# Kernel tuning notes

Hardware: AMD Instinct MI355X
Metric: run time of the kernel (lower is better)

The kernel has to match this reference:

```python
import jax, jax.numpy as jnp
import numpy as np

NUM_GRAPHS = 512  # batch_size (number of segments)


def setup_inputs() -> dict:
    key = jax.random.key(0)
    k1, k2 = jax.random.split(key)
    x = jax.random.normal(k1, (200000, 256), dtype=jnp.float32)
    batch = jnp.sort(jax.random.randint(k2, (200000,), 0, NUM_GRAPHS, dtype=jnp.int64))
    return {"x": x, "batch": batch}


def reference(x, batch):
    # scatter-add node features into per-graph sums: out[g] = sum_{i: batch[i]==g} x[i]
    return jax.ops.segment_sum(x, batch, num_segments=NUM_GRAPHS)
```

## Files before the change

kernel.cpp:

```cpp
#include <hip/hip_runtime.h>


#define FEAT 256
#define F4   (FEAT / 4)
#define NSEG 512

__global__ void seg_bounds_kernel(const int* __restrict__ batch,
                                  int* __restrict__ start, int n) {
    int r = blockIdx.x * blockDim.x + threadIdx.x;
    if (r >= n) return;
    int cur = batch[r];
    if (r == 0) {
        for (int g = 0; g <= cur; ++g) start[g] = 0;
    } else {
        int prev = batch[r - 1];
        for (int g = prev + 1; g <= cur; ++g) start[g] = r;
    }
    if (r == n - 1) {
        for (int g = cur + 1; g <= NSEG; ++g) start[g] = n;
    }
}

__global__ __launch_bounds__(256) void GraphAddPooling_39539468927441_kernel(
    const float* __restrict__ x, const int* __restrict__ start,
    float* __restrict__ out)
{
    const int g    = blockIdx.x;
    const int lane = threadIdx.x & 63;
    const int wave = threadIdx.x >> 6;

    const int r0 = start[g];
    const int r1 = start[g + 1];

    const float4* __restrict__ x4 = (const float4*)x;

    float4 a0 = make_float4(0.f, 0.f, 0.f, 0.f);
    float4 a1 = a0, a2 = a0, a3 = a0;

    int r = r0 + wave;
    for (; r + 12 < r1; r += 16) {
        float4 v0 = x4[(size_t)r        * F4 + lane];
        float4 v1 = x4[(size_t)(r + 4)  * F4 + lane];
        float4 v2 = x4[(size_t)(r + 8)  * F4 + lane];
        float4 v3 = x4[(size_t)(r + 12) * F4 + lane];
        a0.x += v0.x; a0.y += v0.y; a0.z += v0.z; a0.w += v0.w;
        a1.x += v1.x; a1.y += v1.y; a1.z += v1.z; a1.w += v1.w;
        a2.x += v2.x; a2.y += v2.y; a2.z += v2.z; a2.w += v2.w;
        a3.x += v3.x; a3.y += v3.y; a3.z += v3.z; a3.w += v3.w;
    }
    for (; r < r1; r += 4) {
        float4 v = x4[(size_t)r * F4 + lane];
        a0.x += v.x; a0.y += v.y; a0.z += v.z; a0.w += v.w;
    }
    a0.x += a1.x + a2.x + a3.x;
    a0.y += a1.y + a2.y + a3.y;
    a0.z += a1.z + a2.z + a3.z;
    a0.w += a1.w + a2.w + a3.w;

    __shared__ float4 red[4][F4];
    red[wave][lane] = a0;
    __syncthreads();
    if (wave == 0) {
        float4 s = red[0][lane];
        float4 b = red[1][lane], c = red[2][lane], d = red[3][lane];
        s.x += b.x + c.x + d.x;
        s.y += b.y + c.y + d.y;
        s.z += b.z + c.z + d.z;
        s.w += b.w + c.w + d.w;
        ((float4*)out)[(size_t)g * F4 + lane] = s;
    }
}

extern "C" void kernel_launch(void* const* d_in, const int* in_sizes, int n_in,
                              void* d_out, int out_size, void* d_ws, size_t ws_size,
                              hipStream_t stream) {
    const float* x     = (const float*)d_in[0];
    const int*   batch = (const int*)d_in[1];
    float*       out   = (float*)d_out;
    int*         start = (int*)d_ws;

    const int n_rows = in_sizes[1];

    seg_bounds_kernel<<<(n_rows + 255) / 256, 256, 0, stream>>>(batch, start, n_rows);
    GraphAddPooling_39539468927441_kernel<<<NSEG, 256, 0, stream>>>(x, start, out);
}
```

Measured before the change: 282.0 us.

## Split rows evenly across blocks and combine segment partials with atomics

Replaces the one-block-per-segment schedule with a fixed grid of 1024 blocks, each covering an equal contiguous range of rows. Within its range a block walks the segments it overlaps and accumulates each one per wave, adding the partial sums into the output with float atomics after zeroing the output with a memset. The aim is balanced work and more blocks in flight than the 512 segments allowed. In exchange it adds a memset, atomic traffic (four atomics per lane per wave per segment), and a summation order that is no longer deterministic.

```diff
diff --git a/kernel.cpp b/kernel.cpp
--- a/kernel.cpp
+++ b/kernel.cpp
@@ -4,6 +4,7 @@
 #define FEAT 256
 #define F4   (FEAT / 4)
 #define NSEG 512
+#define NB   1024
 
 __global__ void seg_bounds_kernel(const int* __restrict__ batch,
                                   int* __restrict__ start, int n) {
@@ -22,52 +23,56 @@
 }
 
 __global__ __launch_bounds__(256) void GraphAddPooling_39539468927441_kernel(
-    const float* __restrict__ x, const int* __restrict__ start,
-    float* __restrict__ out)
+    const float* __restrict__ x, const int* __restrict__ batch,
+    const int* __restrict__ start, float* __restrict__ out,
+    int n, int rows_per_block)
 {
-    const int g    = blockIdx.x;
     const int lane = threadIdx.x & 63;
     const int wave = threadIdx.x >> 6;
 
-    const int r0 = start[g];
-    const int r1 = start[g + 1];
+    const int c0 = blockIdx.x * rows_per_block;
+    if (c0 >= n) return;
+    int c1 = c0 + rows_per_block;
+    if (c1 > n) c1 = n;
 
     const float4* __restrict__ x4 = (const float4*)x;
 
-    float4 a0 = make_float4(0.f, 0.f, 0.f, 0.f);
-    float4 a1 = a0, a2 = a0, a3 = a0;
+    int g = batch[c0];
+    int r = c0;
+    while (r < c1) {
+        while (start[g + 1] <= r) ++g;
+        int rend = start[g + 1];
+        if (rend > c1) rend = c1;
 
-    int r = r0 + wave;
-    for (; r + 12 < r1; r += 16) {
-        float4 v0 = x4[(size_t)r        * F4 + lane];
-        float4 v1 = x4[(size_t)(r + 4)  * F4 + lane];
-        float4 v2 = x4[(size_t)(r + 8)  * F4 + lane];
-        float4 v3 = x4[(size_t)(r + 12) * F4 + lane];
-        a0.x += v0.x; a0.y += v0.y; a0.z += v0.z; a0.w += v0.w;
-        a1.x += v1.x; a1.y += v1.y; a1.z += v1.z; a1.w += v1.w;
-        a2.x += v2.x; a2.y += v2.y; a2.z += v2.z; a2.w += v2.w;
-        a3.x += v3.x; a3.y += v3.y; a3.z += v3.z; a3.w += v3.w;
-    }
-    for (; r < r1; r += 4) {
-        float4 v = x4[(size_t)r * F4 + lane];
-        a0.x += v.x; a0.y += v.y; a0.z += v.z; a0.w += v.w;
-    }
-    a0.x += a1.x + a2.x + a3.x;
-    a0.y += a1.y + a2.y + a3.y;
-    a0.z += a1.z + a2.z + a3.z;
-    a0.w += a1.w + a2.w + a3.w;
+        float4 a0 = make_float4(0.f, 0.f, 0.f, 0.f);
+        float4 a1 = a0, a2 = a0, a3 = a0;
+        int rr = r + wave;
+        for (; rr + 12 < rend; rr += 16) {
+            float4 v0 = x4[(size_t)rr        * F4 + lane];
+            float4 v1 = x4[(size_t)(rr + 4)  * F4 + lane];
+            float4 v2 = x4[(size_t)(rr + 8)  * F4 + lane];
+            float4 v3 = x4[(size_t)(rr + 12) * F4 + lane];
+            a0.x += v0.x; a0.y += v0.y; a0.z += v0.z; a0.w += v0.w;
+            a1.x += v1.x; a1.y += v1.y; a1.z += v1.z; a1.w += v1.w;
+            a2.x += v2.x; a2.y += v2.y; a2.z += v2.z; a2.w += v2.w;
+            a3.x += v3.x; a3.y += v3.y; a3.z += v3.z; a3.w += v3.w;
+        }
+        for (; rr < rend; rr += 4) {
+            float4 v = x4[(size_t)rr * F4 + lane];
+            a0.x += v.x; a0.y += v.y; a0.z += v.z; a0.w += v.w;
+        }
+        a0.x += a1.x + a2.x + a3.x;
+        a0.y += a1.y + a2.y + a3.y;
+        a0.z += a1.z + a2.z + a3.z;
+        a0.w += a1.w + a2.w + a3.w;
 
-    __shared__ float4 red[4][F4];
-    red[wave][lane] = a0;
-    __syncthreads();
-    if (wave == 0) {
-        float4 s = red[0][lane];
-        float4 b = red[1][lane], c = red[2][lane], d = red[3][lane];
-        s.x += b.x + c.x + d.x;
-        s.y += b.y + c.y + d.y;
-        s.z += b.z + c.z + d.z;
-        s.w += b.w + c.w + d.w;
-        ((float4*)out)[(size_t)g * F4 + lane] = s;
+        float* o = out + (size_t)g * FEAT + lane * 4;
+        atomicAdd(o + 0, a0.x);
+        atomicAdd(o + 1, a0.y);
+        atomicAdd(o + 2, a0.z);
+        atomicAdd(o + 3, a0.w);
+
+        r = rend;
     }
 }
 
@@ -81,6 +86,10 @@
 
     const int n_rows = in_sizes[1];
 
+    hipMemsetAsync(d_out, 0, (size_t)out_size * sizeof(float), stream);
     seg_bounds_kernel<<<(n_rows + 255) / 256, 256, 0, stream>>>(batch, start, n_rows);
-    GraphAddPooling_39539468927441_kernel<<<NSEG, 256, 0, stream>>>(x, start, out);
+
+    const int rows_per_block = (n_rows + NB - 1) / NB;
+    GraphAddPooling_39539468927441_kernel<<<NB, 256, 0, stream>>>(
+        x, batch, start, out, n_rows, rows_per_block);
 }
```

New measurement: 288.4 us. 2.3% more time.
